# Kernel tuning notes

Hardware: AMD Instinct MI355X
Metric: run time of the kernel (lower is better)

Reference implementation:

```python
import jax, jax.numpy as jnp
import numpy as np

B = 32768   # batch
F = 32      # per-node feature dim
H = 256     # hidden width
M = 4       # modules per node
OUT = 8     # final output dim
INIT_W = 0.003
B_INIT = 0.1


def _lin(k, din, dout):
    # fanin_init-style uniform weights, bias filled with 0.1 (hidden layers)
    s = 1.0 / np.sqrt(din)
    W = jax.random.uniform(k, (M, din, dout), jnp.float32, -s, s)
    b = jnp.full((M, dout), B_INIT, jnp.float32)
    return W, b


def setup_inputs() -> dict:
    key = jax.random.key(0)
    ks = jax.random.split(key, 16)
    feats = jax.random.normal(ks[0], (B, 4 * F), jnp.float32)
    idx = jax.random.randint(ks[1], (B, 4), 0, M)
    onehots = jax.nn.one_hot(idx, M, dtype=jnp.float32).reshape(B, 4 * M)
    input_val = jnp.concatenate([feats, onehots], axis=1)  # [B,144]

    W00, b00 = _lin(ks[2], F, H)        # node0 post layer 0
    W01, b01 = _lin(ks[3], H, H)        # node0 post layer 1
    Wpre1, bpre1 = _lin(ks[4], F, H)    # node1 pre
    Wpost1, bpost1 = _lin(ks[5], 2 * H, H)  # node1 interface (prev 256 + own 256)
    Wpre2, bpre2 = _lin(ks[6], F, H)
    Wpost2, bpost2 = _lin(ks[7], 2 * H, H)
    Wpre3, bpre3 = _lin(ks[8], F, H)
    Wpost3, bpost3 = _lin(ks[9], 2 * H, H)
    # final output layer: uniform(-init_w, init_w) for W and b, identity act
    Wfin3 = jax.random.uniform(ks[10], (M, H, OUT), jnp.float32, -INIT_W, INIT_W)
    bfin3 = jax.random.uniform(ks[11], (M, OUT), jnp.float32, -INIT_W, INIT_W)
    return dict(input_val=input_val,
                W00=W00, b00=b00, W01=W01, b01=b01,
                Wpre1=Wpre1, bpre1=bpre1, Wpost1=Wpost1, bpost1=bpost1,
                Wpre2=Wpre2, bpre2=bpre2, Wpost2=Wpost2, bpost2=bpost2,
                Wpre3=Wpre3, bpre3=bpre3, Wpost3=Wpost3, bpost3=bpost3,
                Wfin3=Wfin3, bfin3=bfin3)


def _select(h, onehot):
    # per-row pick of the assigned module's output: [B,M,D],[B,M] -> [B,D]
    return jnp.einsum('bmo,bm->bo', h, onehot)


def reference(input_val, W00, b00, W01, b01,
              Wpre1, bpre1, Wpost1, bpost1,
              Wpre2, bpre2, Wpost2, bpost2,
              Wpre3, bpre3, Wpost3, bpost3,
              Wfin3, bfin3):
    feat = lambda j: input_val[:, j * F:(j + 1) * F]
    oh = lambda j: input_val[:, 4 * F + j * M: 4 * F + (j + 1) * M]

    # node 0: two hidden layers, module-dispatched (dense-all-modules + one-hot combine)
    h = jax.nn.relu(jnp.einsum('bi,mio->bmo', feat(0), W00) + b00)
    h = jax.nn.relu(jnp.einsum('bmi,mio->bmo', h, W01) + b01)
    x = _select(h, oh(0))  # [B,H]

    def node(x_prev, fj, ohj, Wpre, bpre, Wpost, bpost):
        hp = jax.nn.relu(jnp.einsum('bi,mio->bmo', fj, Wpre) + bpre)
        # interface layer consumes concat([x_prev, hp]); split the weight to
        # avoid materializing [B,M,2H]
        hq = jax.nn.relu(jnp.einsum('bi,mio->bmo', x_prev, Wpost[:, :H, :])
                         + jnp.einsum('bmi,mio->bmo', hp, Wpost[:, H:, :])
                         + bpost)
        return hq  # [B,M,H]

    x = _select(node(x, feat(1), oh(1), Wpre1, bpre1, Wpost1, bpost1), oh(1))
    x = _select(node(x, feat(2), oh(2), Wpre2, bpre2, Wpost2, bpost2), oh(2))

    h3 = node(x, feat(3), oh(3), Wpre3, bpre3, Wpost3, bpost3)  # [B,M,H]
    out = jnp.einsum('bmi,mio->bmo', h3, Wfin3) + bfin3          # final linear, identity act
    return _select(out, oh(3))  # [B,OUT]
```

## Files before the change

### kernel.cpp

```cpp
#include <hip/hip_runtime.h>

#define NB 32768
#define MAXTILE 768
#define ROWS 64
#define NT 4
#define XHS 536

typedef short s8v __attribute__((ext_vector_type(8)));
typedef short s4v __attribute__((ext_vector_type(4)));
typedef float f4v __attribute__((ext_vector_type(4)));
typedef unsigned short u16;
typedef unsigned short u16x4 __attribute__((ext_vector_type(4)));
typedef unsigned int u32;
typedef unsigned char u8;

__device__ __forceinline__ float bf2f(u16 u) { return __uint_as_float(((u32)u) << 16); }
__device__ __forceinline__ u16 f2bf(float f) {
    u32 x = __float_as_uint(f);
    x += 0x7FFFu + ((x >> 16) & 1u);
    return (u16)(x >> 16);
}
__device__ __forceinline__ s8v ld8(const u16* p) { return *reinterpret_cast<const s8v*>(p); }

#define MFMA16(a, b, c) __builtin_amdgcn_mfma_f32_16x16x32_bf16((a), (b), (c), 0, 0, 0)

template <int N> struct IC { static constexpr int v = N; };

__device__ __forceinline__ void detect_flag(const void* input, int tid, int* shflag)
{
    if (tid < 64) {
        u32 w = ((const u32*)input)[tid];
        u32 h0 = w & 0xFFFFu;
        u32 e0 = (h0 >> 7) & 0xFFu;
        bool plaus = (h0 == 0u) || (e0 >= 96u && e0 <= 143u);
        unsigned long long m = __ballot(plaus);
        if (tid == 0) *shflag = (__popcll(m) >= 48) ? 1 : 0;
    }
}

struct RepArgs {
    const void* W01; const void* Wp[3]; const void* pre[4]; const void* fin;
    const void* bias[9];
    u16 *rPre, *rW01, *rWp[3], *rFin, *cbias;
};

__global__ __launch_bounds__(256) void prepA_kernel(const void* __restrict__ inputv,
                                                    int* __restrict__ hist,
                                                    u16* __restrict__ keyloc,
                                                    RepArgs R)
{
    __shared__ int lcnt[256];
    __shared__ u16 T[8192];
    __shared__ int shmisc;
    int tid = threadIdx.x;
    int b = blockIdx.x;
    detect_flag(inputv, tid, &shmisc);
    __syncthreads();
    int flag = shmisc;

    if (b < 128) {
        lcnt[tid] = 0;
        __syncthreads();
        int row = (b << 8) + tid;
        const u32* in32 = (const u32*)inputv;
        const u16* in16 = (const u16*)inputv;
        int key = 0;
#pragma unroll
        for (int j = 0; j < 4; j++) {
            int base = row * 144 + 128 + j * 4;
            u32 v1, v2, v3;
            if (flag) { v1 = in16[base + 1]; v2 = in16[base + 2]; v3 = in16[base + 3]; }
            else      { v1 = in32[base + 1]; v2 = in32[base + 2]; v3 = in32[base + 3]; }
            int m = v1 ? 1 : (v2 ? 2 : (v3 ? 3 : 0));
            key |= m << (j << 1);
        }
        int loc = atomicAdd(&lcnt[key], 1);
        keyloc[row] = (u16)(key | (loc << 8));
        __syncthreads();
        hist[(b << 8) + tid] = lcnt[tid];
        return;
    }

    int rb = b - 128;
    const void* src = nullptr; u16* dst = nullptr; int K = 0, k0 = 0, mrow = 0;
    if (rb < 32) {
        int m = rb >> 3, s = rb & 7;
        src = R.W01; dst = R.rW01 + (m * 8 + s) * 8192; K = 256; k0 = s * 32; mrow = m;
    } else if (rb < 224) {
        int idx = rb - 32, mat = idx >> 6, r = idx & 63, m = r >> 4, s = r & 15;
        src = R.Wp[mat]; dst = R.rWp[mat] + (m * 16 + s) * 8192; K = 512; k0 = s * 32; mrow = m;
    } else if (rb < 240) {
        int idx = rb - 224, mat = idx >> 2, m = idx & 3;
        src = R.pre[mat]; dst = R.rPre + (mat * 4 + m) * 8192; K = 32; k0 = 0; mrow = m;
    } else if (rb < 244) {
        int m = rb - 240;
        const u16* s16 = (const u16*)R.fin;
        const float* s32 = (const float*)R.fin;
        for (int i = tid; i < 2048; i += 256) {
            int si = (m * 256 + (i >> 3)) * 8 + (i & 7);
            T[i] = flag ? s16[si] : f2bf(s32[si]);
        }
        __syncthreads();
        u16* d = R.rFin + m * 4096;
        for (int i = tid; i < 4096; i += 256) {
            int s = i >> 9, lane = (i >> 3) & 63, j = i & 7;
            int q = lane >> 4, l16 = lane & 15;
            int k = s * 32 + q * 8 + j;
            d[i] = (l16 < 8) ? T[k * 8 + l16] : (u16)0;
        }
        return;
    } else {
        const int sz[9] = {1024,1024,1024,1024,1024,1024,1024,1024,32};
        const int of[9] = {0,1024,2048,3072,4096,5120,6144,7168,8192};
        for (int i = tid; i < 8224; i += 256) {
            int t = i, e = 0;
            while (t >= sz[e]) { t -= sz[e]; e++; }
            R.cbias[of[e] + t] = flag ? ((const u16*)R.bias[e])[t]
                                      : f2bf(((const float*)R.bias[e])[t]);
        }
        return;
    }
    const u16* s16 = (const u16*)src;
    const float* s32 = (const float*)src;
    for (int i = tid; i < 8192; i += 256) {
        int k = i >> 8, n = i & 255;
        int srcIdx = (mrow * K + k0 + k) * 256 + n;
        T[i] = flag ? s16[srcIdx] : f2bf(s32[srcIdx]);
    }
    __syncthreads();
    for (int i = tid; i < 8192; i += 256) {
        int mt = i >> 9, lane = (i >> 3) & 63, j = i & 7;
        int k = ((lane >> 4) << 3) + j, n = (mt << 4) + (lane & 15);
        dst[i] = T[(k << 8) + n];
    }
}

__global__ __launch_bounds__(256) void scatter_kernel(const void* __restrict__ inputv,
                                                      const int* __restrict__ hist,
                                                      const u16* __restrict__ keyloc,
                                                      int* __restrict__ perm,
                                                      u16* __restrict__ sortedFeats,
                                                      int4* __restrict__ tileInfo)
{
    __shared__ int lcnt[256];
    __shared__ int sBase[256];
    __shared__ int shflag;
    int tid = threadIdx.x;
    int b = blockIdx.x;
    detect_flag(inputv, tid, &shflag);
    __syncthreads();
    int flag = shflag;

    int before = 0, tot = 0;
    for (int b2 = 0; b2 < 128; b2++) {
        int h = hist[(b2 << 8) + tid];
        tot += h;
        if (b2 < b) before += h;
    }
    lcnt[tid] = tot;
    __syncthreads();
    for (int off = 1; off < 256; off <<= 1) {
        int v = (tid >= off) ? lcnt[tid - off] : 0;
        __syncthreads();
        lcnt[tid] += v;
        __syncthreads();
    }
    int gbase = lcnt[tid] - tot;
    sBase[tid] = gbase + before;
    __syncthreads();

    if (b == 0) {
        int tiles = (tot + ROWS - 1) / ROWS;
        lcnt[tid] = tiles;
        __syncthreads();
        for (int off = 1; off < 256; off <<= 1) {
            int v = (tid >= off) ? lcnt[tid - off] : 0;
            __syncthreads();
            lcnt[tid] += v;
            __syncthreads();
        }
        int tbase = lcnt[tid] - tiles;
        int ttot = lcnt[255];
        for (int t = 0; t < tiles; t++) {
            int rem = tot - t * ROWS;
            tileInfo[tbase + t] = make_int4(tid, gbase + t * ROWS, rem > ROWS ? ROWS : rem, 0);
        }
        for (int i = ttot + tid; i < MAXTILE; i += 256)
            tileInfo[i] = make_int4(0, 0, 0, 0);
    }

    int row = (b << 8) + tid;
    u32 kl = keyloc[row];
    int key = kl & 255, loc = kl >> 8;
    int dst = sBase[key] + loc;
    perm[dst] = row;
    u16* d = sortedFeats + (size_t)dst * 128;
    if (flag) {
        const u16* s = (const u16*)inputv + row * 144;
#pragma unroll
        for (int i = 0; i < 128; i += 8)
            *(s8v*)(d + i) = *(const s8v*)(s + i);
    } else {
        const float* s = (const float*)inputv + row * 144;
#pragma unroll
        for (int i = 0; i < 128; i += 4) {
            f4v f = *(const f4v*)(s + i);
            s4v p;
#pragma unroll
            for (int r = 0; r < 4; r++) p[r] = (short)f2bf(f[r]);
            *(s4v*)(d + i) = p;
        }
    }
}

struct MainP { const u16 *rPre, *rW01, *rWp1, *rWp2, *rWp3, *rFin, *cbias; };

__global__ __launch_bounds__(512, 4) void main_kernel(
    const void* __restrict__ inRaw, const u16* __restrict__ sortedFeats,
    const int* __restrict__ perm, const int4* __restrict__ tileInfo,
    MainP P, void* __restrict__ outp)
{
    __shared__ __align__(16) u16 xh[ROWS * XHS];
    __shared__ int rowids[ROWS];
    __shared__ int shflag;

    int tid = threadIdx.x;
    int lane = tid & 63, w = tid >> 6, quad = lane >> 4, l16 = lane & 15;

    int4 ti = tileInfo[blockIdx.x];
    int key = ti.x, ppos = ti.y, cntIn = ti.z;
    if (cntIn <= 0) return;

    detect_flag(inRaw, tid, &shflag);
    if (tid < ROWS) {
        int g = tid < cntIn ? tid : cntIn - 1;
        rowids[tid] = perm[ppos + g];
    }
    __syncthreads();
    int flag = shflag;
    int fidx[NT];
#pragma unroll
    for (int nt = 0; nt < NT; nt++) {
        int gi = ppos + nt * 16 + l16;
        fidx[nt] = gi < NB ? gi : NB - 1;
    }
    int mt0 = w << 1, mt1 = mt0 + 1;

    f4v acc0[NT], acc1[NT];

    auto gemm_run = [&](auto nc, const u16* Ab, int ks0) {
        constexpr int N = decltype(nc)::v;
        constexpr int D = 4;
        const u16* base0 = Ab + mt0 * 512 + lane * 8;
        const u16* base1 = Ab + mt1 * 512 + lane * 8;
        s8v A0[D], A1[D];
#pragma unroll
        for (int d = 0; d < D && d < N; d++) {
            A0[d] = ld8(base0 + d * 8192);
            A1[d] = ld8(base1 + d * 8192);
        }
        __syncthreads();
#pragma unroll
        for (int s = 0; s < N; s++) {
            s8v c0 = A0[s % D], c1 = A1[s % D];
            if (s + D < N) {
                A0[s % D] = ld8(base0 + (s + D) * 8192);
                A1[s % D] = ld8(base1 + (s + D) * 8192);
            }
#pragma unroll
            for (int nt = 0; nt < NT; nt++) {
                s8v B = ld8(&xh[(nt * 16 + l16) * XHS + (ks0 + s) * 32 + quad * 8]);
                acc0[nt] = MFMA16(c0, B, acc0[nt]);
                acc1[nt] = MFMA16(c1, B, acc1[nt]);
            }
        }
    };

    for (int node = 0; node < 4; node++) {
        int m = (key >> (node << 1)) & 3;

        s8v fb[NT];
#pragma unroll
        for (int nt = 0; nt < NT; nt++)
            fb[nt] = ld8(sortedFeats + (size_t)fidx[nt] * 128 + (node << 5) + (quad << 3));

        const u16* preB = P.rPre + ((node << 2) + m) * 8192;
#pragma unroll
        for (int ci = 0; ci < 2; ci++) {
            int mt = mt0 + ci;
            s8v a = ld8(preB + mt * 512 + lane * 8);
            u16x4 bv = *(const u16x4*)(P.cbias + node * 2048 + m * 256 + mt * 16 + quad * 4);
            f4v bias;
#pragma unroll
            for (int r = 0; r < 4; r++) bias[r] = bf2f(bv[r]);
#pragma unroll
            for (int nt = 0; nt < NT; nt++) {
                f4v c = MFMA16(a, fb[nt], bias);
                s4v p;
#pragma unroll
                for (int r = 0; r < 4; r++) { float v = c[r] > 0.f ? c[r] : 0.f; p[r] = (short)f2bf(v); }
                *(s4v*)&xh[(nt * 16 + l16) * XHS + 256 + mt * 16 + quad * 4] = p;
            }
        }

        {
            u16x4 b0 = *(const u16x4*)(P.cbias + node * 2048 + 1024 + m * 256 + mt0 * 16 + quad * 4);
            u16x4 b1 = *(const u16x4*)(P.cbias + node * 2048 + 1024 + m * 256 + mt1 * 16 + quad * 4);
            f4v f0, f1;
#pragma unroll
            for (int r = 0; r < 4; r++) { f0[r] = bf2f(b0[r]); f1[r] = bf2f(b1[r]); }
#pragma unroll
            for (int nt = 0; nt < NT; nt++) { acc0[nt] = f0; acc1[nt] = f1; }
        }

        if (node == 0) gemm_run(IC<8>{},  P.rW01 + m * 8 * 8192, 8);
        else {
            const u16* WB = (node == 1 ? P.rWp1 : (node == 2 ? P.rWp2 : P.rWp3)) + m * 16 * 8192;
            gemm_run(IC<16>{}, WB, 0);
        }
        __syncthreads();

#pragma unroll
        for (int ci = 0; ci < 2; ci++) {
            int mt = mt0 + ci;
#pragma unroll
            for (int nt = 0; nt < NT; nt++) {
                f4v a = ci ? acc1[nt] : acc0[nt];
                s4v p;
#pragma unroll
                for (int r = 0; r < 4; r++) { float v = a[r] > 0.f ? a[r] : 0.f; p[r] = (short)f2bf(v); }
                *(s4v*)&xh[(nt * 16 + l16) * XHS + mt * 16 + quad * 4] = p;
            }
        }
    }
    __syncthreads();

    if (w < NT) {
        int m3 = (key >> 6) & 3;
        f4v c;
#pragma unroll
        for (int r = 0; r < 4; r++)
            c[r] = (quad < 2) ? bf2f(P.cbias[8192 + m3 * 8 + quad * 4 + r]) : 0.f;
#pragma unroll
        for (int s = 0; s < 8; s++) {
            s8v A = ld8(P.rFin + m3 * 4096 + s * 512 + lane * 8);
            s8v B = ld8(&xh[(w * 16 + l16) * XHS + s * 32 + quad * 8]);
            c = MFMA16(A, B, c);
        }
        int bidx = w * 16 + l16;
        if (quad < 2 && bidx < cntIn) {
            int row = rowids[bidx];
            if (flag) {
                s4v p;
#pragma unroll
                for (int r = 0; r < 4; r++) p[r] = (short)f2bf(c[r]);
                *(s4v*)((u16*)outp + row * 8 + quad * 4) = p;
            } else {
                *(f4v*)((float*)outp + row * 8 + quad * 4) = c;
            }
        }
    }
}

extern "C" void kernel_launch(void* const* d_in, const int* in_sizes, int n_in,
                              void* d_out, int out_size, void* d_ws, size_t ws_size,
                              hipStream_t stream)
{
    (void)in_sizes; (void)n_in; (void)out_size;
    const void* input  = d_in[0];
    const void* W00    = d_in[1];
    const void* b00    = d_in[2];
    const void* W01    = d_in[3];
    const void* b01    = d_in[4];
    const void* Wpre1  = d_in[5];
    const void* bpre1  = d_in[6];
    const void* Wpost1 = d_in[7];
    const void* bpost1 = d_in[8];
    const void* Wpre2  = d_in[9];
    const void* bpre2  = d_in[10];
    const void* Wpost2 = d_in[11];
    const void* bpost2 = d_in[12];
    const void* Wpre3  = d_in[13];
    const void* bpre3  = d_in[14];
    const void* Wpost3 = d_in[15];
    const void* bpost3 = d_in[16];
    const void* Wfin   = d_in[17];
    const void* bfin   = d_in[18];

    char* base = (char*)d_ws;
    size_t off = 0;
    auto alloc = [&](size_t bytes) -> char* {
        char* p = base + off;
        off += (bytes + 255) & ~(size_t)255;
        return p;
    };
    int*  hist      = (int*)alloc(128 * 256 * 4);
    u16*  keyloc    = (u16*)alloc(NB * 2);
    int4* tileInfo  = (int4*)alloc(MAXTILE * 16);
    int*  perm      = (int*)alloc((size_t)NB * 4);
    u16*  sortedFeats = (u16*)alloc((size_t)NB * 128 * 2);
    u16*  cbias    = (u16*)alloc(8224 * 2);
    u16*  rPre     = (u16*)alloc(131072 * 2);
    u16*  rW01     = (u16*)alloc(262144 * 2);
    u16*  rWp1     = (u16*)alloc(524288 * 2);
    u16*  rWp2     = (u16*)alloc(524288 * 2);
    u16*  rWp3     = (u16*)alloc(524288 * 2);
    u16*  rFin     = (u16*)alloc(16384 * 2);
    if (off > ws_size) return;

    RepArgs R;
    R.W01 = W01; R.Wp[0] = Wpost1; R.Wp[1] = Wpost2; R.Wp[2] = Wpost3;
    R.pre[0] = W00; R.pre[1] = Wpre1; R.pre[2] = Wpre2; R.pre[3] = Wpre3;
    R.fin = Wfin;
    R.bias[0] = b00;   R.bias[1] = b01;
    R.bias[2] = bpre1; R.bias[3] = bpost1;
    R.bias[4] = bpre2; R.bias[5] = bpost2;
    R.bias[6] = bpre3; R.bias[7] = bpost3;
    R.bias[8] = bfin;
    R.rPre = rPre; R.rW01 = rW01;
    R.rWp[0] = rWp1; R.rWp[1] = rWp2; R.rWp[2] = rWp3;
    R.rFin = rFin; R.cbias = cbias;

    prepA_kernel<<<373, 256, 0, stream>>>(input, hist, keyloc, R);
    scatter_kernel<<<128, 256, 0, stream>>>(input, hist, keyloc, perm, sortedFeats, tileInfo);

    MainP P;
    P.rPre = rPre; P.rW01 = rW01; P.rWp1 = rWp1; P.rWp2 = rWp2; P.rWp3 = rWp3;
    P.rFin = rFin; P.cbias = cbias;
    main_kernel<<<MAXTILE, 512, 0, stream>>>(input, sortedFeats, perm, tileInfo, P, d_out);
}
```

Before: 203.1 us.

## Gather features directly from input in main kernel, drop sorted feature copy

```diff
diff --git a/kernel.cpp b/kernel.cpp
--- a/kernel.cpp
+++ b/kernel.cpp
@@ -135,21 +135,15 @@
     }
 }
 
-__global__ __launch_bounds__(256) void scatter_kernel(const void* __restrict__ inputv,
-                                                      const int* __restrict__ hist,
+__global__ __launch_bounds__(256) void scatter_kernel(const int* __restrict__ hist,
                                                       const u16* __restrict__ keyloc,
                                                       int* __restrict__ perm,
-                                                      u16* __restrict__ sortedFeats,
                                                       int4* __restrict__ tileInfo)
 {
     __shared__ int lcnt[256];
     __shared__ int sBase[256];
-    __shared__ int shflag;
     int tid = threadIdx.x;
     int b = blockIdx.x;
-    detect_flag(inputv, tid, &shflag);
-    __syncthreads();
-    int flag = shflag;
 
     int before = 0, tot = 0;
     for (int b2 = 0; b2 < 128; b2++) {
@@ -192,31 +186,13 @@
     int row = (b << 8) + tid;
     u32 kl = keyloc[row];
     int key = kl & 255, loc = kl >> 8;
-    int dst = sBase[key] + loc;
-    perm[dst] = row;
-    u16* d = sortedFeats + (size_t)dst * 128;
-    if (flag) {
-        const u16* s = (const u16*)inputv + row * 144;
-#pragma unroll
-        for (int i = 0; i < 128; i += 8)
-            *(s8v*)(d + i) = *(const s8v*)(s + i);
-    } else {
-        const float* s = (const float*)inputv + row * 144;
-#pragma unroll
-        for (int i = 0; i < 128; i += 4) {
-            f4v f = *(const f4v*)(s + i);
-            s4v p;
-#pragma unroll
-            for (int r = 0; r < 4; r++) p[r] = (short)f2bf(f[r]);
-            *(s4v*)(d + i) = p;
-        }
-    }
+    perm[sBase[key] + loc] = row;
 }
 
 struct MainP { const u16 *rPre, *rW01, *rWp1, *rWp2, *rWp3, *rFin, *cbias; };
 
 __global__ __launch_bounds__(512, 4) void main_kernel(
-    const void* __restrict__ inRaw, const u16* __restrict__ sortedFeats,
+    const void* __restrict__ inRaw,
     const int* __restrict__ perm, const int4* __restrict__ tileInfo,
     MainP P, void* __restrict__ outp)
 {
@@ -227,7 +203,9 @@
     int tid = threadIdx.x;
     int lane = tid & 63, w = tid >> 6, quad = lane >> 4, l16 = lane & 15;
 
-    int4 ti = tileInfo[blockIdx.x];
+    int b = blockIdx.x;
+    int t = ((b & 7) * (MAXTILE / 8)) + (b >> 3);
+    int4 ti = tileInfo[t];
     int key = ti.x, ppos = ti.y, cntIn = ti.z;
     if (cntIn <= 0) return;
 
@@ -238,12 +216,12 @@
     }
     __syncthreads();
     int flag = shflag;
-    int fidx[NT];
-#pragma unroll
-    for (int nt = 0; nt < NT; nt++) {
-        int gi = ppos + nt * 16 + l16;
-        fidx[nt] = gi < NB ? gi : NB - 1;
-    }
+    int rows_[NT];
+#pragma unroll
+    for (int nt = 0; nt < NT; nt++) rows_[nt] = rowids[nt * 16 + l16];
+
+    const u16* in16 = (const u16*)inRaw;
+    const float* in32 = (const float*)inRaw;
     int mt0 = w << 1, mt1 = mt0 + 1;
 
     f4v acc0[NT], acc1[NT];
@@ -281,8 +259,18 @@
 
         s8v fb[NT];
 #pragma unroll
-        for (int nt = 0; nt < NT; nt++)
-            fb[nt] = ld8(sortedFeats + (size_t)fidx[nt] * 128 + (node << 5) + (quad << 3));
+        for (int nt = 0; nt < NT; nt++) {
+            int off = rows_[nt] * 144 + (node << 5) + (quad << 3);
+            if (flag) fb[nt] = ld8(in16 + off);
+            else {
+                f4v f0 = *(const f4v*)(in32 + off);
+                f4v f1 = *(const f4v*)(in32 + off + 4);
+                s8v r;
+#pragma unroll
+                for (int j = 0; j < 4; j++) { r[j] = (short)f2bf(f0[j]); r[4 + j] = (short)f2bf(f1[j]); }
+                fb[nt] = r;
+            }
+        }
 
         const u16* preB = P.rPre + ((node << 2) + m) * 8192;
 #pragma unroll
@@ -398,7 +386,6 @@
     u16*  keyloc    = (u16*)alloc(NB * 2);
     int4* tileInfo  = (int4*)alloc(MAXTILE * 16);
     int*  perm      = (int*)alloc((size_t)NB * 4);
-    u16*  sortedFeats = (u16*)alloc((size_t)NB * 128 * 2);
     u16*  cbias    = (u16*)alloc(8224 * 2);
     u16*  rPre     = (u16*)alloc(131072 * 2);
     u16*  rW01     = (u16*)alloc(262144 * 2);
@@ -422,10 +409,10 @@
     R.rFin = rFin; R.cbias = cbias;
 
     prepA_kernel<<<373, 256, 0, stream>>>(input, hist, keyloc, R);
-    scatter_kernel<<<128, 256, 0, stream>>>(input, hist, keyloc, perm, sortedFeats, tileInfo);
+    scatter_kernel<<<128, 256, 0, stream>>>(hist, keyloc, perm, tileInfo);
 
     MainP P;
     P.rPre = rPre; P.rW01 = rW01; P.rWp1 = rWp1; P.rWp2 = rWp2; P.rWp3 = rWp3;
     P.rFin = rFin; P.cbias = cbias;
-    main_kernel<<<MAXTILE, 512, 0, stream>>>(input, sortedFeats, perm, tileInfo, P, d_out);
-}
+    main_kernel<<<MAXTILE, 512, 0, stream>>>(input, perm, tileInfo, P, d_out);
+}
```

Result: faster. 194.5 us (-4.2%).
